# Performance work log

Hardware: AMD Instinct MI355X
Metric: run time of the kernel (lower is better)

The kernel has to match this reference:

```python
import jax, jax.numpy as jnp
import numpy as np

N = 6144          # nodes
F_IN = 512        # num_feature
HID = 64          # hidden_dim
C = 40            # num_class
H = 3             # num_heads
ALPHA = 0.2       # leaky relu slope
NEG_INF = -9e15


def gat_layer(x, adj, W, a_src, a_dst):
    # x: [N, f_in], W: [H, f_in, f_out], a_src/a_dst: [H, f_out]
    Wh = jnp.einsum('nf,hfo->hno', x, W)                  # [H, N, f_out]
    e_src = jnp.einsum('hno,ho->hn', Wh, a_src)           # [H, N]
    e_dst = jnp.einsum('hno,ho->hn', Wh, a_dst)           # [H, N]
    e = jax.nn.leaky_relu(e_src[:, :, None] + e_dst[:, None, :], ALPHA)  # [H, N, N]
    scores = jnp.where(adj > 0, e, NEG_INF)               # mask non-edges
    attn = jax.nn.softmax(scores, axis=-1)                # softmax over neighbors
    out = jnp.einsum('hnm,hmo->hno', attn, Wh)            # [H, N, f_out]
    return out.mean(axis=0)                               # average heads -> [N, f_out]


def setup_inputs() -> dict:
    key = jax.random.key(0)
    k = jax.random.split(key, 8)
    feature = jax.random.normal(k[0], (N, F_IN), dtype=jnp.float32)
    adj = (jax.random.uniform(k[1], (N, N)) < 0.01).astype(jnp.float32)
    adj = jnp.maximum(adj, jnp.eye(N, dtype=jnp.float32))
    s1 = 1.0 / np.sqrt(F_IN)
    s2 = 1.0 / np.sqrt(HID)
    W1 = jax.random.normal(k[2], (H, F_IN, HID), dtype=jnp.float32) * s1
    a1_src = jax.random.normal(k[3], (H, HID), dtype=jnp.float32) * s2
    a1_dst = jax.random.normal(k[4], (H, HID), dtype=jnp.float32) * s2
    W2 = jax.random.normal(k[5], (H, HID, C), dtype=jnp.float32) * s2
    a2_src = jax.random.normal(k[6], (H, C), dtype=jnp.float32) * (1.0 / np.sqrt(C))
    a2_dst = jax.random.normal(k[7], (H, C), dtype=jnp.float32) * (1.0 / np.sqrt(C))
    return {"feature": feature, "adj": adj, "W1": W1, "a1_src": a1_src,
            "a1_dst": a1_dst, "W2": W2, "a2_src": a2_src, "a2_dst": a2_dst}


def reference(feature, adj, W1, a1_src, a1_dst, W2, a2_src, a2_dst):
    # eval mode: dropout is identity
    x = jax.nn.relu(gat_layer(feature, adj, W1, a1_src, a1_dst))  # [N, HID]
    x = gat_layer(x, adj, W2, a2_src, a2_dst)                     # [N, C]
    return jax.nn.log_softmax(x, axis=1)
```

## Files before the change

kernel.cpp:

```cpp
#include <hip/hip_runtime.h>
#include <math.h>

#define NN   6144
#define FIN  512
#define HIDN 64
#define NC   40
#define NH   3
#define CAP  128
#define NCHUNK (CAP / 64)
#define LALPHA 0.2f
#define KSPLIT 4
#define PK_LOW  0x3FFFu
#define PK_HIGH 0xFFFFC000u
#define NGRP   (NN * NN / 256)
#define GPW    18
#define CSRB   (NN / 4)

typedef unsigned long long ull;

__device__ __forceinline__ float bf2f(ushort s) {
    return __uint_as_float((unsigned)s << 16);
}
__device__ __forceinline__ ushort f2bf(float f) {
    unsigned u = __float_as_uint(f);
    return (ushort)((u + 0x7FFFu + ((u >> 16) & 1u)) >> 16);
}

__global__ __launch_bounds__(256) void k_bits(const float* __restrict__ adj,
                                              ull* __restrict__ bits) {
    int gwid = (blockIdx.x * 256 + (int)threadIdx.x) >> 6;
    int lane = threadIdx.x & 63;
    const float* p = adj + (size_t)gwid * GPW * 256 + lane * 4;
    ull* bp = bits + (size_t)gwid * GPW * 4;
    for (int t = 0; t < 3; t++) {
        float4 v[6];
#pragma unroll
        for (int i = 0; i < 6; i++)
            v[i] = *reinterpret_cast<const float4*>(p + (t * 6 + i) * 256);
#pragma unroll
        for (int i = 0; i < 6; i++) {
            ull b0 = __ballot(v[i].x > 0.f);
            ull b1 = __ballot(v[i].y > 0.f);
            ull b2 = __ballot(v[i].z > 0.f);
            ull b3 = __ballot(v[i].w > 0.f);
            if (lane == 0) {
                ulonglong2* q = reinterpret_cast<ulonglong2*>(bp + (size_t)(t * 6 + i) * 4);
                ulonglong2 w0; w0.x = b0; w0.y = b1;
                ulonglong2 w1; w1.x = b2; w1.y = b3;
                q[0] = w0; q[1] = w1;
            }
        }
    }
}

__global__ __launch_bounds__(256) void k_gemm1(const float* __restrict__ x,
                                               const float* __restrict__ W,
                                               float* __restrict__ Whp) {
    __shared__ float xs[64][68];
    __shared__ float wsh[64][68];
    int h  = blockIdx.y;
    int n0 = blockIdx.x * 64;
    int kz = blockIdx.z;
    int tid = threadIdx.x;
    int og4 = (tid & 15) * 4;
    int mg4 = (tid >> 4) * 4;

    float acc[4][4] = {{0.f}};
    const float* xbase0 = x + (size_t)n0 * FIN;
    const float* wbase0 = W + (size_t)h * FIN * HIDN;

    for (int t = 0; t < 2; t++) {
        int k0 = kz * 128 + t * 64;
#pragma unroll
        for (int i = 0; i < 4; i++) {
            int l = tid + i * 256;
            int r = l >> 4;
            int c = (l & 15) * 4;
            *reinterpret_cast<float4*>(&xs[r][c]) =
                *reinterpret_cast<const float4*>(xbase0 + (size_t)r * FIN + k0 + c);
            *reinterpret_cast<float4*>(&wsh[r][c]) =
                *reinterpret_cast<const float4*>(wbase0 + (size_t)(k0 + r) * HIDN + c);
        }
        __syncthreads();

#pragma unroll 8
        for (int k = 0; k < 64; k += 4) {
            float4 xv[4], wv[4];
            xv[0] = *reinterpret_cast<const float4*>(&xs[mg4 + 0][k]);
            xv[1] = *reinterpret_cast<const float4*>(&xs[mg4 + 1][k]);
            xv[2] = *reinterpret_cast<const float4*>(&xs[mg4 + 2][k]);
            xv[3] = *reinterpret_cast<const float4*>(&xs[mg4 + 3][k]);
            wv[0] = *reinterpret_cast<const float4*>(&wsh[k + 0][og4]);
            wv[1] = *reinterpret_cast<const float4*>(&wsh[k + 1][og4]);
            wv[2] = *reinterpret_cast<const float4*>(&wsh[k + 2][og4]);
            wv[3] = *reinterpret_cast<const float4*>(&wsh[k + 3][og4]);
            const float* xf = reinterpret_cast<const float*>(xv);
            const float* wf = reinterpret_cast<const float*>(wv);
#pragma unroll
            for (int i = 0; i < 4; i++) {
#pragma unroll
                for (int kk = 0; kk < 4; kk++) {
                    float xval = xf[i * 4 + kk];
#pragma unroll
                    for (int j = 0; j < 4; j++)
                        acc[i][j] += xval * wf[kk * 4 + j];
                }
            }
        }
        __syncthreads();
    }

    float* outp = Whp + (((size_t)kz * NH + h) * NN + n0 + mg4) * HIDN + og4;
#pragma unroll
    for (int i = 0; i < 4; i++) {
        float4 v = make_float4(acc[i][0], acc[i][1], acc[i][2], acc[i][3]);
        *reinterpret_cast<float4*>(outp + (size_t)i * HIDN) = v;
    }
}

__global__ __launch_bounds__(256) void k_csr2_sume1(const ull* __restrict__ bits,
                                                    int* __restrict__ nbr,
                                                    int* __restrict__ deg,
                                                    const float* __restrict__ Whp,
                                                    const float* __restrict__ a_src,
                                                    const float* __restrict__ a_dst,
                                                    ushort* __restrict__ Whb,
                                                    float* __restrict__ es,
                                                    float* __restrict__ ed) {
    int lane = threadIdx.x & 63;
    if (blockIdx.x < CSRB) {
        int row = blockIdx.x * 4 + ((int)threadIdx.x >> 6);
        const ull* brow = bits + (size_t)row * 96;
        int W0 = lane, W1 = 64 + lane;
        ull m0 = brow[W0];
        ull m1 = (lane < 32) ? brow[W1] : 0ull;
        int c0 = __popcll(m0), c1 = __popcll(m1);
        int s0 = c0, s1 = c1;
#pragma unroll
        for (int off = 1; off < 64; off <<= 1) {
            int t0 = __shfl_up(s0, off);
            int t1 = __shfl_up(s1, off);
            if (lane >= off) { s0 += t0; s1 += t1; }
        }
        int total0 = __shfl(s0, 63);
        int total  = total0 + __shfl(s1, 63);
        int pre0 = s0 - c0;
        int pre1 = total0 + (s1 - c1);
        if (lane == 0) deg[row] = total < CAP ? total : CAP;
        int* nrow = nbr + (size_t)row * CAP;
        int g0 = (W0 >> 2) * 256 + (W0 & 3);
        int pos = pre0;
        while (m0) {
            int b = __builtin_ctzll(m0); m0 &= m0 - 1;
            if (pos < CAP) nrow[pos] = g0 + 4 * b;
            pos++;
        }
        int g1 = (W1 >> 2) * 256 + (W1 & 3);
        pos = pre1;
        while (m1) {
            int b = __builtin_ctzll(m1); m1 &= m1 - 1;
            if (pos < CAP) nrow[pos] = g1 + 4 * b;
            pos++;
        }
        return;
    }
    int gw = (blockIdx.x - CSRB) * 4 + ((int)threadIdx.x >> 6);
    int h = gw / NN, n = gw % NN;
    size_t idx = ((size_t)h * NN + n) * HIDN + lane;
    size_t stride = (size_t)NH * NN * HIDN;
    float v = Whp[idx] + Whp[idx + stride] + Whp[idx + 2 * stride] + Whp[idx + 3 * stride];
    Whb[idx] = f2bf(v);
    float s = v * a_src[h * HIDN + lane];
    float d = v * a_dst[h * HIDN + lane];
#pragma unroll
    for (int off = 32; off; off >>= 1) {
        s += __shfl_xor(s, off);
        d += __shfl_xor(d, off);
    }
    if (lane == 0) { es[h * NN + n] = s; ed[h * NN + n] = d; }
}

__global__ __launch_bounds__(192) void k_attn1f(const int* __restrict__ nbr,
                                                const int* __restrict__ deg,
                                                const ushort* __restrict__ Whb,
                                                const float* __restrict__ es,
                                                const float* __restrict__ ed,
                                                const float* __restrict__ W2,
                                                const float* __restrict__ a2s,
                                                const float* __restrict__ a2d,
                                                ushort* __restrict__ Wh2b,
                                                float* __restrict__ e2s,
                                                float* __restrict__ e2d) {
    __shared__ unsigned pks[NH][CAP];
    __shared__ float hsum[NH][HIDN];
    int n = blockIdx.x;
    int h = threadIdx.x >> 6;
    int lane = threadIdx.x & 63;
    int d = deg[n];
    const int* nrow = nbr + (size_t)n * CAP;
    float esv = es[h * NN + n];

    float psum = 0.f;
#pragma unroll
    for (int c = 0; c < NCHUNK; c++) {
        int k = c * 64 + lane;
        unsigned u = 0;
        if (k < d) {
            int mm = nrow[k];
            float e = esv + ed[h * NN + mm];
            float s = e > 0.f ? e : LALPHA * e;
            float p = __expf(s);
            u = (__float_as_uint(p) & PK_HIGH) | (unsigned)mm;
            psum += __uint_as_float(u & PK_HIGH);
        }
        pks[h][k] = u;
    }
#pragma unroll
    for (int off = 32; off; off >>= 1) psum += __shfl_xor(psum, off);
    float inv = 1.f / psum;
    __syncthreads();

    const ushort* WhH = Whb + (size_t)h * NN * HIDN + lane;
    float a0 = 0.f, a1 = 0.f, a2 = 0.f, a3 = 0.f;
    int iters = (d + 3) >> 2;
    for (int g = 0; g < iters; g++) {
        uint4 uu = *reinterpret_cast<const uint4*>(&pks[h][g * 4]);
        a0 += __uint_as_float(uu.x & PK_HIGH) * bf2f(WhH[(size_t)(uu.x & PK_LOW) * HIDN]);
        a1 += __uint_as_float(uu.y & PK_HIGH) * bf2f(WhH[(size_t)(uu.y & PK_LOW) * HIDN]);
        a2 += __uint_as_float(uu.z & PK_HIGH) * bf2f(WhH[(size_t)(uu.z & PK_LOW) * HIDN]);
        a3 += __uint_as_float(uu.w & PK_HIGH) * bf2f(WhH[(size_t)(uu.w & PK_LOW) * HIDN]);
    }
    float hacc = ((a0 + a1) + (a2 + a3));
    hsum[h][lane] = hacc * inv;
    __syncthreads();

    float xv = (hsum[0][lane] + hsum[1][lane] + hsum[2][lane]) * (1.f / NH);
    xv = fmaxf(xv, 0.f);

    int c = lane < NC ? lane : NC - 1;
    float acc = 0.f;
#pragma unroll 8
    for (int o = 0; o < HIDN; o++) {
        float xb = __shfl(xv, o);
        float wv = W2[((size_t)h * HIDN + o) * NC + c];
        acc += xb * wv;
    }
    if (lane >= NC) acc = 0.f;

    float s2 = acc * (lane < NC ? a2s[h * NC + lane] : 0.f);
    float d2 = acc * (lane < NC ? a2d[h * NC + lane] : 0.f);
#pragma unroll
    for (int off = 32; off; off >>= 1) {
        s2 += __shfl_xor(s2, off);
        d2 += __shfl_xor(d2, off);
    }
    if (lane < NC) Wh2b[((size_t)h * NN + n) * NC + lane] = f2bf(acc);
    if (lane == 0) { e2s[h * NN + n] = s2; e2d[h * NN + n] = d2; }
}

__global__ __launch_bounds__(192) void k_attn2(const int* __restrict__ nbr,
                                               const int* __restrict__ deg,
                                               const ushort* __restrict__ Wh2b,
                                               const float* __restrict__ es,
                                               const float* __restrict__ ed,
                                               float* __restrict__ out) {
    __shared__ unsigned pks[NH][CAP];
    __shared__ float hsum[NH][HIDN];
    int n = blockIdx.x;
    int h = threadIdx.x >> 6;
    int lane = threadIdx.x & 63;
    int d = deg[n];
    const int* nrow = nbr + (size_t)n * CAP;
    float esv = es[h * NN + n];

    float psum = 0.f;
#pragma unroll
    for (int c = 0; c < NCHUNK; c++) {
        int k = c * 64 + lane;
        unsigned u = 0;
        if (k < d) {
            int mm = nrow[k];
            float e = esv + ed[h * NN + mm];
            float s = e > 0.f ? e : LALPHA * e;
            float p = __expf(s);
            u = (__float_as_uint(p) & PK_HIGH) | (unsigned)mm;
            psum += __uint_as_float(u & PK_HIGH);
        }
        pks[h][k] = u;
    }
#pragma unroll
    for (int off = 32; off; off >>= 1) psum += __shfl_xor(psum, off);
    float inv = 1.f / psum;
    __syncthreads();

    const ushort* W2H = Wh2b + (size_t)h * NN * NC + (lane < NC ? lane : 0);
    float a0 = 0.f, a1 = 0.f, a2 = 0.f, a3 = 0.f;
    int iters = (d + 3) >> 2;
    for (int g = 0; g < iters; g++) {
        uint4 uu = *reinterpret_cast<const uint4*>(&pks[h][g * 4]);
        a0 += __uint_as_float(uu.x & PK_HIGH) * bf2f(W2H[(size_t)(uu.x & PK_LOW) * NC]);
        a1 += __uint_as_float(uu.y & PK_HIGH) * bf2f(W2H[(size_t)(uu.y & PK_LOW) * NC]);
        a2 += __uint_as_float(uu.z & PK_HIGH) * bf2f(W2H[(size_t)(uu.z & PK_LOW) * NC]);
        a3 += __uint_as_float(uu.w & PK_HIGH) * bf2f(W2H[(size_t)(uu.w & PK_LOW) * NC]);
    }
    float hacc = ((a0 + a1) + (a2 + a3));
    if (lane < NC) hsum[h][lane] = hacc * inv;
    __syncthreads();

    if (threadIdx.x < 64) {
        float a = (lane < NC)
            ? (hsum[0][lane] + hsum[1][lane] + hsum[2][lane]) * (1.f / NH)
            : -INFINITY;
        float mx = a;
#pragma unroll
        for (int off = 32; off; off >>= 1) mx = fmaxf(mx, __shfl_xor(mx, off));
        float ex = (lane < NC) ? __expf(a - mx) : 0.f;
        float se = ex;
#pragma unroll
        for (int off = 32; off; off >>= 1) se += __shfl_xor(se, off);
        if (lane < NC) out[(size_t)n * NC + lane] = a - mx - logf(se);
    }
}

extern "C" void kernel_launch(void* const* d_in, const int* in_sizes, int n_in,
                              void* d_out, int out_size, void* d_ws, size_t ws_size,
                              hipStream_t stream) {
    const float* feature = (const float*)d_in[0];
    const float* adj     = (const float*)d_in[1];
    const float* W1      = (const float*)d_in[2];
    const float* a1_src  = (const float*)d_in[3];
    const float* a1_dst  = (const float*)d_in[4];
    const float* W2      = (const float*)d_in[5];
    const float* a2_src  = (const float*)d_in[6];
    const float* a2_dst  = (const float*)d_in[7];
    float* out = (float*)d_out;

    char* ws = (char*)d_ws;
    size_t off = 0;
    ull*    bits = (ull*)(ws + off);   off += (size_t)NGRP * 4 * sizeof(ull);
    int*    nbr = (int*)(ws + off);    off += (size_t)NN * CAP * sizeof(int);
    int*    deg = (int*)(ws + off);    off += (size_t)NN * sizeof(int);
    float*  Whp = (float*)(ws + off);  off += (size_t)KSPLIT * NH * NN * HIDN * sizeof(float);
    ushort* Whb = (ushort*)(ws + off); off += (size_t)NH * NN * HIDN * sizeof(ushort);
    float*  e1s = (float*)(ws + off);  off += (size_t)NH * NN * sizeof(float);
    float*  e1d = (float*)(ws + off);  off += (size_t)NH * NN * sizeof(float);
    ushort* Wh2b= (ushort*)(ws + off); off += (size_t)NH * NN * NC * sizeof(ushort);
    float*  e2s = (float*)(ws + off);  off += (size_t)NH * NN * sizeof(float);
    float*  e2d = (float*)(ws + off);  off += (size_t)NH * NN * sizeof(float);

    k_bits<<<2048, 256, 0, stream>>>(adj, bits);
    k_gemm1<<<dim3(NN / 64, NH, KSPLIT), 256, 0, stream>>>(feature, W1, Whp);
    k_csr2_sume1<<<CSRB + (NH * NN) / 4, 256, 0, stream>>>(bits, nbr, deg, Whp,
                                                           a1_src, a1_dst, Whb, e1s, e1d);
    k_attn1f<<<NN, 192, 0, stream>>>(nbr, deg, Whb, e1s, e1d, W2, a2_src, a2_dst,
                                     Wh2b, e2s, e2d);
    k_attn2<<<NN, 192, 0, stream>>>(nbr, deg, Wh2b, e2s, e2d, out);
}
```

Measured before the change: 103.8 us.

## Fuse adjacency bitpack with full-K GEMM and build CSR inside attention kernel

Merges the adjacency bit-packing kernel and the first-layer GEMM into one launch, with GEMM blocks interleaved among bitpack blocks. The GEMM now runs the full K without a split, writing bf16 Wh and the attention logits directly, which removes the fp32 partial buffer and the separate reduction pass. The per-row CSR build moves into the first attention kernel through shared memory, which drops one launch and its global round-trip. In exchange, the GEMM grid shrinks to 288 blocks that each run a longer serial K loop, and the attention kernel does extra serial work on one wavefront before its barrier.

```diff
diff --git a/kernel.cpp b/kernel.cpp
--- a/kernel.cpp
+++ b/kernel.cpp
@@ -9,12 +9,13 @@
 #define CAP  128
 #define NCHUNK (CAP / 64)
 #define LALPHA 0.2f
-#define KSPLIT 4
 #define PK_LOW  0x3FFFu
 #define PK_HIGH 0xFFFFC000u
 #define NGRP   (NN * NN / 256)
 #define GPW    18
-#define CSRB   (NN / 4)
+#define GEMMB  ((NN / 64) * NH)
+#define BITSB  2048
+#define TOTB   (BITSB + GEMMB)
 
 typedef unsigned long long ull;
 
@@ -26,51 +27,65 @@
     return (ushort)((u + 0x7FFFu + ((u >> 16) & 1u)) >> 16);
 }
 
-__global__ __launch_bounds__(256) void k_bits(const float* __restrict__ adj,
-                                              ull* __restrict__ bits) {
-    int gwid = (blockIdx.x * 256 + (int)threadIdx.x) >> 6;
-    int lane = threadIdx.x & 63;
-    const float* p = adj + (size_t)gwid * GPW * 256 + lane * 4;
-    ull* bp = bits + (size_t)gwid * GPW * 4;
-    for (int t = 0; t < 3; t++) {
-        float4 v[6];
-#pragma unroll
-        for (int i = 0; i < 6; i++)
-            v[i] = *reinterpret_cast<const float4*>(p + (t * 6 + i) * 256);
-#pragma unroll
-        for (int i = 0; i < 6; i++) {
-            ull b0 = __ballot(v[i].x > 0.f);
-            ull b1 = __ballot(v[i].y > 0.f);
-            ull b2 = __ballot(v[i].z > 0.f);
-            ull b3 = __ballot(v[i].w > 0.f);
-            if (lane == 0) {
-                ulonglong2* q = reinterpret_cast<ulonglong2*>(bp + (size_t)(t * 6 + i) * 4);
-                ulonglong2 w0; w0.x = b0; w0.y = b1;
-                ulonglong2 w1; w1.x = b2; w1.y = b3;
-                q[0] = w0; q[1] = w1;
+__global__ __launch_bounds__(256) void k_bits_gemm(const float* __restrict__ adj,
+                                                   ull* __restrict__ bits,
+                                                   const float* __restrict__ x,
+                                                   const float* __restrict__ W,
+                                                   const float* __restrict__ a_src,
+                                                   const float* __restrict__ a_dst,
+                                                   ushort* __restrict__ Whb,
+                                                   float* __restrict__ es,
+                                                   float* __restrict__ ed) {
+    __shared__ float smem[2 * 64 * 68];
+    int bid = blockIdx.x;
+    int tid = threadIdx.x;
+    int lane = tid & 63;
+    int pg = bid >> 3;
+    bool isGemm = ((bid & 7) == 7) && (pg < GEMMB);
+
+    if (!isGemm) {
+        int prior = pg < GEMMB ? pg : GEMMB;
+        int bi = bid - prior;
+        int gwid = bi * 4 + (tid >> 6);
+        const float* p = adj + (size_t)gwid * GPW * 256 + lane * 4;
+        ull* bp = bits + (size_t)gwid * GPW * 4;
+        for (int t = 0; t < 3; t++) {
+            float4 v[6];
+#pragma unroll
+            for (int i = 0; i < 6; i++)
+                v[i] = *reinterpret_cast<const float4*>(p + (t * 6 + i) * 256);
+#pragma unroll
+            for (int i = 0; i < 6; i++) {
+                ull b0 = __ballot(v[i].x > 0.f);
+                ull b1 = __ballot(v[i].y > 0.f);
+                ull b2 = __ballot(v[i].z > 0.f);
+                ull b3 = __ballot(v[i].w > 0.f);
+                if (lane == 0) {
+                    ulonglong2* q = reinterpret_cast<ulonglong2*>(bp + (size_t)(t * 6 + i) * 4);
+                    ulonglong2 w0; w0.x = b0; w0.y = b1;
+                    ulonglong2 w1; w1.x = b2; w1.y = b3;
+                    q[0] = w0; q[1] = w1;
+                }
             }
         }
-    }
-}
-
-__global__ __launch_bounds__(256) void k_gemm1(const float* __restrict__ x,
-                                               const float* __restrict__ W,
-                                               float* __restrict__ Whp) {
-    __shared__ float xs[64][68];
-    __shared__ float wsh[64][68];
-    int h  = blockIdx.y;
-    int n0 = blockIdx.x * 64;
-    int kz = blockIdx.z;
-    int tid = threadIdx.x;
+        return;
+    }
+
+    int gb = pg;
+    int h  = gb / (NN / 64);
+    int n0 = (gb % (NN / 64)) * 64;
     int og4 = (tid & 15) * 4;
     int mg4 = (tid >> 4) * 4;
+
+    float (*xs)[68]  = reinterpret_cast<float(*)[68]>(smem);
+    float (*wsh)[68] = reinterpret_cast<float(*)[68]>(smem + 64 * 68);
 
     float acc[4][4] = {{0.f}};
     const float* xbase0 = x + (size_t)n0 * FIN;
     const float* wbase0 = W + (size_t)h * FIN * HIDN;
 
-    for (int t = 0; t < 2; t++) {
-        int k0 = kz * 128 + t * 64;
+    for (int t = 0; t < 8; t++) {
+        int k0 = t * 64;
 #pragma unroll
         for (int i = 0; i < 4; i++) {
             int l = tid + i * 256;
@@ -110,78 +125,46 @@
         __syncthreads();
     }
 
-    float* outp = Whp + (((size_t)kz * NH + h) * NN + n0 + mg4) * HIDN + og4;
+    size_t rowbase = (size_t)h * NN + n0 + mg4;
 #pragma unroll
     for (int i = 0; i < 4; i++) {
-        float4 v = make_float4(acc[i][0], acc[i][1], acc[i][2], acc[i][3]);
-        *reinterpret_cast<float4*>(outp + (size_t)i * HIDN) = v;
-    }
-}
-
-__global__ __launch_bounds__(256) void k_csr2_sume1(const ull* __restrict__ bits,
-                                                    int* __restrict__ nbr,
-                                                    int* __restrict__ deg,
-                                                    const float* __restrict__ Whp,
-                                                    const float* __restrict__ a_src,
-                                                    const float* __restrict__ a_dst,
-                                                    ushort* __restrict__ Whb,
-                                                    float* __restrict__ es,
-                                                    float* __restrict__ ed) {
-    int lane = threadIdx.x & 63;
-    if (blockIdx.x < CSRB) {
-        int row = blockIdx.x * 4 + ((int)threadIdx.x >> 6);
-        const ull* brow = bits + (size_t)row * 96;
-        int W0 = lane, W1 = 64 + lane;
-        ull m0 = brow[W0];
-        ull m1 = (lane < 32) ? brow[W1] : 0ull;
-        int c0 = __popcll(m0), c1 = __popcll(m1);
-        int s0 = c0, s1 = c1;
-#pragma unroll
-        for (int off = 1; off < 64; off <<= 1) {
-            int t0 = __shfl_up(s0, off);
-            int t1 = __shfl_up(s1, off);
-            if (lane >= off) { s0 += t0; s1 += t1; }
-        }
-        int total0 = __shfl(s0, 63);
-        int total  = total0 + __shfl(s1, 63);
-        int pre0 = s0 - c0;
-        int pre1 = total0 + (s1 - c1);
-        if (lane == 0) deg[row] = total < CAP ? total : CAP;
-        int* nrow = nbr + (size_t)row * CAP;
-        int g0 = (W0 >> 2) * 256 + (W0 & 3);
-        int pos = pre0;
-        while (m0) {
-            int b = __builtin_ctzll(m0); m0 &= m0 - 1;
-            if (pos < CAP) nrow[pos] = g0 + 4 * b;
-            pos++;
-        }
-        int g1 = (W1 >> 2) * 256 + (W1 & 3);
-        pos = pre1;
-        while (m1) {
-            int b = __builtin_ctzll(m1); m1 &= m1 - 1;
-            if (pos < CAP) nrow[pos] = g1 + 4 * b;
-            pos++;
-        }
-        return;
-    }
-    int gw = (blockIdx.x - CSRB) * 4 + ((int)threadIdx.x >> 6);
-    int h = gw / NN, n = gw % NN;
-    size_t idx = ((size_t)h * NN + n) * HIDN + lane;
-    size_t stride = (size_t)NH * NN * HIDN;
-    float v = Whp[idx] + Whp[idx + stride] + Whp[idx + 2 * stride] + Whp[idx + 3 * stride];
-    Whb[idx] = f2bf(v);
-    float s = v * a_src[h * HIDN + lane];
-    float d = v * a_dst[h * HIDN + lane];
-#pragma unroll
-    for (int off = 32; off; off >>= 1) {
-        s += __shfl_xor(s, off);
-        d += __shfl_xor(d, off);
-    }
-    if (lane == 0) { es[h * NN + n] = s; ed[h * NN + n] = d; }
-}
-
-__global__ __launch_bounds__(192) void k_attn1f(const int* __restrict__ nbr,
-                                                const int* __restrict__ deg,
+        ushort4 b;
+        b.x = f2bf(acc[i][0]); b.y = f2bf(acc[i][1]);
+        b.z = f2bf(acc[i][2]); b.w = f2bf(acc[i][3]);
+        *reinterpret_cast<ushort4*>(Whb + (rowbase + i) * HIDN + og4) = b;
+    }
+    float as4[4], ad4[4];
+#pragma unroll
+    for (int j = 0; j < 4; j++) {
+        as4[j] = a_src[h * HIDN + og4 + j];
+        ad4[j] = a_dst[h * HIDN + og4 + j];
+    }
+    float se[4], de[4];
+#pragma unroll
+    for (int i = 0; i < 4; i++) {
+        se[i] = acc[i][0] * as4[0] + acc[i][1] * as4[1] + acc[i][2] * as4[2] + acc[i][3] * as4[3];
+        de[i] = acc[i][0] * ad4[0] + acc[i][1] * ad4[1] + acc[i][2] * ad4[2] + acc[i][3] * ad4[3];
+    }
+#pragma unroll
+    for (int off = 1; off < 16; off <<= 1) {
+#pragma unroll
+        for (int i = 0; i < 4; i++) {
+            se[i] += __shfl_xor(se[i], off);
+            de[i] += __shfl_xor(de[i], off);
+        }
+    }
+    if ((tid & 15) == 0) {
+#pragma unroll
+        for (int i = 0; i < 4; i++) {
+            es[rowbase + i] = se[i];
+            ed[rowbase + i] = de[i];
+        }
+    }
+}
+
+__global__ __launch_bounds__(192) void k_attn1f(const ull* __restrict__ bits,
+                                                int* __restrict__ nbr,
+                                                int* __restrict__ deg,
                                                 const ushort* __restrict__ Whb,
                                                 const float* __restrict__ es,
                                                 const float* __restrict__ ed,
@@ -191,22 +174,61 @@
                                                 ushort* __restrict__ Wh2b,
                                                 float* __restrict__ e2s,
                                                 float* __restrict__ e2d) {
+    __shared__ int nbrL[CAP];
+    __shared__ int degS;
     __shared__ unsigned pks[NH][CAP];
     __shared__ float hsum[NH][HIDN];
     int n = blockIdx.x;
     int h = threadIdx.x >> 6;
     int lane = threadIdx.x & 63;
-    int d = deg[n];
-    const int* nrow = nbr + (size_t)n * CAP;
+
+    if (h == 0) {
+        const ull* brow = bits + (size_t)n * 96;
+        int W0 = lane, W1 = 64 + lane;
+        ull m0 = brow[W0];
+        ull m1 = (lane < 32) ? brow[W1] : 0ull;
+        int c0 = __popcll(m0), c1 = __popcll(m1);
+        int s0 = c0, s1 = c1;
+#pragma unroll
+        for (int off = 1; off < 64; off <<= 1) {
+            int t0 = __shfl_up(s0, off);
+            int t1 = __shfl_up(s1, off);
+            if (lane >= off) { s0 += t0; s1 += t1; }
+        }
+        int total0 = __shfl(s0, 63);
+        int total  = total0 + __shfl(s1, 63);
+        int pre0 = s0 - c0;
+        int pre1 = total0 + (s1 - c1);
+        if (lane == 0) degS = total < CAP ? total : CAP;
+        int g0 = (W0 >> 2) * 256 + (W0 & 3);
+        int pos = pre0;
+        while (m0) {
+            int b = __builtin_ctzll(m0); m0 &= m0 - 1;
+            if (pos < CAP) nbrL[pos] = g0 + 4 * b;
+            pos++;
+        }
+        int g1 = (W1 >> 2) * 256 + (W1 & 3);
+        pos = pre1;
+        while (m1) {
+            int b = __builtin_ctzll(m1); m1 &= m1 - 1;
+            if (pos < CAP) nbrL[pos] = g1 + 4 * b;
+            pos++;
+        }
+    }
+    __syncthreads();
+    int d = degS;
+    if (threadIdx.x < CAP)
+        nbr[(size_t)n * CAP + threadIdx.x] = ((int)threadIdx.x < d) ? nbrL[threadIdx.x] : 0;
+    if (threadIdx.x == 0) deg[n] = d;
+
     float esv = es[h * NN + n];
-
     float psum = 0.f;
 #pragma unroll
     for (int c = 0; c < NCHUNK; c++) {
         int k = c * 64 + lane;
         unsigned u = 0;
         if (k < d) {
-            int mm = nrow[k];
+            int mm = nbrL[k];
             float e = esv + ed[h * NN + mm];
             float s = e > 0.f ? e : LALPHA * e;
             float p = __expf(s);
@@ -340,7 +362,6 @@
     ull*    bits = (ull*)(ws + off);   off += (size_t)NGRP * 4 * sizeof(ull);
     int*    nbr = (int*)(ws + off);    off += (size_t)NN * CAP * sizeof(int);
     int*    deg = (int*)(ws + off);    off += (size_t)NN * sizeof(int);
-    float*  Whp = (float*)(ws + off);  off += (size_t)KSPLIT * NH * NN * HIDN * sizeof(float);
     ushort* Whb = (ushort*)(ws + off); off += (size_t)NH * NN * HIDN * sizeof(ushort);
     float*  e1s = (float*)(ws + off);  off += (size_t)NH * NN * sizeof(float);
     float*  e1d = (float*)(ws + off);  off += (size_t)NH * NN * sizeof(float);
@@ -348,11 +369,9 @@
     float*  e2s = (float*)(ws + off);  off += (size_t)NH * NN * sizeof(float);
     float*  e2d = (float*)(ws + off);  off += (size_t)NH * NN * sizeof(float);
 
-    k_bits<<<2048, 256, 0, stream>>>(adj, bits);
-    k_gemm1<<<dim3(NN / 64, NH, KSPLIT), 256, 0, stream>>>(feature, W1, Whp);
-    k_csr2_sume1<<<CSRB + (NH * NN) / 4, 256, 0, stream>>>(bits, nbr, deg, Whp,
-                                                           a1_src, a1_dst, Whb, e1s, e1d);
-    k_attn1f<<<NN, 192, 0, stream>>>(nbr, deg, Whb, e1s, e1d, W2, a2_src, a2_dst,
+    k_bits_gemm<<<TOTB, 256, 0, stream>>>(adj, bits, feature, W1, a1_src, a1_dst,
+                                          Whb, e1s, e1d);
+    k_attn1f<<<NN, 192, 0, stream>>>(bits, nbr, deg, Whb, e1s, e1d, W2, a2_src, a2_dst,
                                      Wh2b, e2s, e2d);
     k_attn2<<<NN, 192, 0, stream>>>(nbr, deg, Wh2b, e2s, e2d, out);
 }
```

New measurement: 172.3 us. +66.0%, slower.
